# Kernel tuning notes

Measured on AMD Instinct MI355X. Metric: run time of the kernel, lower is better.

## Reference

```python
import jax, jax.numpy as jnp
import numpy as np
import math

B, S, DK, DV = 8, 2048, 128, 128
SQRT_DK = math.sqrt(DK)


def setup_inputs() -> dict:
    key = jax.random.key(0)
    kq, kk, kv = jax.random.split(key, 3)
    Q = jax.random.normal(kq, (B, S, DK), dtype=jnp.float32)
    K = jax.random.normal(kk, (B, S, DK), dtype=jnp.float32)
    V = jax.random.normal(kv, (B, S, DV), dtype=jnp.float32)
    # additive causal mask, broadcast over batch: 0 on/below diag, -1e9 above
    causal = jnp.tril(jnp.ones((S, S), dtype=bool))
    mask = jnp.where(causal, 0.0, -1e9).astype(jnp.float32)[None]  # [1, S, S]
    return {"Q": Q, "K": K, "V": V, "mask": mask}


def reference(Q, K, V, mask):
    # QK = Q @ K^T / sqrt(dk); dropout is identity in eval mode.
    scores = jnp.einsum("bqd,bkd->bqk", Q, K) / SQRT_DK + mask  # [B, S, S]
    # transpose->softmax(dim=1)->transpose == softmax over key axis (last dim)
    A = jax.nn.softmax(scores, axis=-1)
    return jnp.einsum("bqk,bkv->bqv", A, V)  # [B, S, DV]
```

## Files before the change

### kernel.cpp

```cpp
#include <hip/hip_runtime.h>

#define SEQ 2048
#define DHEAD 128
#define NB 8
#define KST 136
#define VST 72
#define PST 72

typedef short short8 __attribute__((ext_vector_type(8)));
typedef float f32x4 __attribute__((ext_vector_type(4)));

__device__ __constant__ unsigned char UNIT[80] = {
    124,125,126,127, 120,121,122, 116,117,118, 112,113,114, 108,109,110,
    104,105,106, 96,97,98, 100,101,102, 92,93,94, 88,89, 84,85, 80,81,
    76,77, 72,73, 68,69, 64,65, 60,61, 56, 52, 48, 44, 40, 36, 32, 28,
    123, 90, 57, 24,
    119, 86, 53, 20,
    115, 82, 49, 16,
    111, 78, 45, 12,
    107, 74, 41,  8,
    103, 70, 37,  4,
     99, 66, 33,  0
};

__device__ __forceinline__ unsigned short f2bf(float x) {
    unsigned int u = __float_as_uint(x);
    u += 0x7fffu + ((u >> 16) & 1u);
    return (unsigned short)(u >> 16);
}

__device__ __forceinline__ float bf2f(unsigned short h) {
    return __uint_as_float(((unsigned int)h) << 16);
}

__global__ void prep(const float* __restrict__ K, const float* __restrict__ V,
                     unsigned short* __restrict__ Kb, unsigned short* __restrict__ Vt) {
    if (blockIdx.x < 2048) {
        int i = blockIdx.x * 256 + threadIdx.x;
        float4 v = ((const float4*)K)[i];
        ushort4 o;
        o.x = f2bf(v.x); o.y = f2bf(v.y); o.z = f2bf(v.z); o.w = f2bf(v.w);
        ((ushort4*)Kb)[i] = o;
    } else {
        __shared__ unsigned short t[32][33];
        int bx = blockIdx.x - 2048;
        int b = bx >> 8, xy = bx & 255;
        int s0 = (xy >> 2) << 5;
        int d0 = (xy & 3) << 5;
        int tid = threadIdx.x;
        int sl = tid >> 3, dl = (tid & 7) << 2;
        float4 v = *(const float4*)&V[(b * SEQ + s0 + sl) * DHEAD + d0 + dl];
        t[sl][dl + 0] = f2bf(v.x); t[sl][dl + 1] = f2bf(v.y);
        t[sl][dl + 2] = f2bf(v.z); t[sl][dl + 3] = f2bf(v.w);
        __syncthreads();
        int dr = tid >> 3, sr = (tid & 7) << 2;
        ushort4 o;
        o.x = t[sr + 0][dr]; o.y = t[sr + 1][dr]; o.z = t[sr + 2][dr]; o.w = t[sr + 3][dr];
        *(ushort4*)&Vt[(b * DHEAD + d0 + dr) * SEQ + s0 + sr] = o;
    }
}

__global__ __launch_bounds__(256, 3)
void flash_attn(const float* __restrict__ Q, const unsigned short* __restrict__ Kb,
                const unsigned short* __restrict__ Vt,
                unsigned short* __restrict__ Opart, float* __restrict__ lsumP,
                float* __restrict__ out) {
    __shared__ __align__(16) unsigned short Klds[64 * KST];
    __shared__ __align__(16) unsigned short Vlds[128 * VST];
    __shared__ __align__(16) unsigned short Pb[4][16 * PST];

    const int b = blockIdx.x & 7;
    const int e = UNIT[blockIdx.x >> 3];
    const int qt = e >> 2, c = e & 3;
    const int kt0 = c * 8;
    const int kt1 = min(qt + 1, kt0 + 8);

    const int tid = threadIdx.x;
    const int w = tid >> 6, lane = tid & 63;
    const int ln15 = lane & 15, g = lane >> 4;
    const int qrow0 = qt * 64 + w * 16;

    const float scale = 0.08838834764831845f;
    short8 qf[4];
    {
        const float* qp = Q + (b * SEQ + qrow0 + ln15) * DHEAD + g * 8;
#pragma unroll
        for (int cc = 0; cc < 4; ++cc) {
            float4 a = *(const float4*)(qp + cc * 32);
            float4 d = *(const float4*)(qp + cc * 32 + 4);
            short8 f;
            f[0] = f2bf(a.x * scale); f[1] = f2bf(a.y * scale);
            f[2] = f2bf(a.z * scale); f[3] = f2bf(a.w * scale);
            f[4] = f2bf(d.x * scale); f[5] = f2bf(d.y * scale);
            f[6] = f2bf(d.z * scale); f[7] = f2bf(d.w * scale);
            qf[cc] = f;
        }
    }

    f32x4 acc[8];
#pragma unroll
    for (int j = 0; j < 8; ++j) acc[j] = (f32x4){0.f, 0.f, 0.f, 0.f};
    float lsum = 0.f;
    unsigned short* P = &Pb[w][0];

    {
        const int k0 = kt0 << 6;
        short8 pre[8];
#pragma unroll
        for (int j = 0; j < 4; ++j) {
            int ck = tid + j * 256;
            pre[j]     = *(const short8*)(Kb + (b * SEQ + k0 + (ck >> 4)) * DHEAD + (ck & 15) * 8);
            pre[4 + j] = *(const short8*)(Vt + (b * DHEAD + (ck >> 3)) * SEQ + k0 + (ck & 7) * 8);
        }
#pragma unroll
        for (int j = 0; j < 4; ++j) {
            int ck = tid + j * 256;
            *(short8*)&Klds[(ck >> 4) * KST + (ck & 15) * 8] = pre[j];
            *(short8*)&Vlds[(ck >> 3) * VST + (ck & 7) * 8]  = pre[4 + j];
        }
    }
    __syncthreads();

    for (int kt = kt0; kt < kt1; ++kt) {
        const int k0 = kt << 6;
        const bool have_next = (kt + 1 < kt1);
        short8 pre2[8];
        if (have_next) {
            const int kn = (kt + 1) << 6;
#pragma unroll
            for (int j = 0; j < 4; ++j) {
                int ck = tid + j * 256;
                pre2[j]     = *(const short8*)(Kb + (b * SEQ + kn + (ck >> 4)) * DHEAD + (ck & 15) * 8);
                pre2[4 + j] = *(const short8*)(Vt + (b * DHEAD + (ck >> 3)) * SEQ + kn + (ck & 7) * 8);
            }
        }

        if (k0 <= qrow0 + 15) {
            const bool nm = (k0 + 63 > qrow0);
#pragma unroll
            for (int mtp = 0; mtp < 2; ++mtp) {
                short8 kf[8];
#pragma unroll
                for (int cc = 0; cc < 4; ++cc) {
                    kf[cc]     = *(const short8*)&Klds[((2 * mtp) * 16 + ln15) * KST + cc * 32 + g * 8];
                    kf[4 + cc] = *(const short8*)&Klds[((2 * mtp + 1) * 16 + ln15) * KST + cc * 32 + g * 8];
                }
                f32x4 s0 = (f32x4){0.f, 0.f, 0.f, 0.f};
                f32x4 s1 = (f32x4){0.f, 0.f, 0.f, 0.f};
#pragma unroll
                for (int cc = 0; cc < 4; ++cc) {
                    s0 = __builtin_amdgcn_mfma_f32_16x16x32_bf16(kf[cc],     qf[cc], s0, 0, 0, 0);
                    s1 = __builtin_amdgcn_mfma_f32_16x16x32_bf16(kf[4 + cc], qf[cc], s1, 0, 0, 0);
                }
#pragma unroll
                for (int h = 0; h < 2; ++h) {
                    f32x4 s = h ? s1 : s0;
                    const int mt = 2 * mtp + h;
                    float p[4];
#pragma unroll
                    for (int r = 0; r < 4; ++r) {
                        p[r] = __expf(s[r]);
                        if (nm) {
                            int colg = k0 + mt * 16 + g * 4 + r;
                            int rowg = qrow0 + ln15;
                            p[r] = (colg <= rowg) ? p[r] : 0.f;
                        }
                    }
                    lsum += (p[0] + p[1]) + (p[2] + p[3]);
                    uint2 dd;
                    dd.x = __builtin_amdgcn_perm(__float_as_uint(p[1]), __float_as_uint(p[0]), 0x07060302u);
                    dd.y = __builtin_amdgcn_perm(__float_as_uint(p[3]), __float_as_uint(p[2]), 0x07060302u);
                    *(uint2*)&P[ln15 * PST + mt * 16 + g * 4] = dd;
                }
            }
#pragma unroll
            for (int c2 = 0; c2 < 2; ++c2) {
                short8 vf[8];
#pragma unroll
                for (int nt2 = 0; nt2 < 8; ++nt2)
                    vf[nt2] = *(const short8*)&Vlds[(nt2 * 16 + ln15) * VST + c2 * 32 + g * 8];
                short8 pf = *(const short8*)&P[ln15 * PST + c2 * 32 + g * 8];
#pragma unroll
                for (int nt2 = 0; nt2 < 8; ++nt2)
                    acc[nt2] = __builtin_amdgcn_mfma_f32_16x16x32_bf16(pf, vf[nt2], acc[nt2], 0, 0, 0);
            }
        }

        if (have_next) {
            __syncthreads();
#pragma unroll
            for (int j = 0; j < 4; ++j) {
                int ck = tid + j * 256;
                *(short8*)&Klds[(ck >> 4) * KST + (ck & 15) * 8] = pre2[j];
                *(short8*)&Vlds[(ck >> 3) * VST + (ck & 7) * 8]  = pre2[4 + j];
            }
            __syncthreads();
        }
    }

    {
        float v = lsum;
        v += __shfl_xor(v, 16);
        v += __shfl_xor(v, 32);
        lsum = v;
    }

    if (qt < 8) {
        float inv[4];
#pragma unroll
        for (int r = 0; r < 4; ++r) inv[r] = 1.0f / __shfl(lsum, g * 4 + r);
#pragma unroll
        for (int nt2 = 0; nt2 < 8; ++nt2) {
#pragma unroll
            for (int r = 0; r < 4; ++r) {
                int rowg = qrow0 + g * 4 + r;
                out[(b * SEQ + rowg) * DHEAD + nt2 * 16 + ln15] = acc[nt2][r] * inv[r];
            }
        }
    } else {
        if (lane < 16)
            lsumP[(c * NB + b) * 1536 + qrow0 + lane - 512] = lsum;
#pragma unroll
        for (int nt2 = 0; nt2 < 8; ++nt2) {
#pragma unroll
            for (int r = 0; r < 4; ++r) {
                int r2 = qrow0 + g * 4 + r - 512;
                Opart[((c * NB + b) * 1536 + r2) * DHEAD + nt2 * 16 + ln15] = f2bf(acc[nt2][r]);
            }
        }
    }
}

__global__ void finalize(const unsigned short* __restrict__ Opart,
                         const float* __restrict__ lsumP, float* __restrict__ out) {
    int b = blockIdx.y;
    int gx = blockIdx.x * 256 + threadIdx.x;
    int d4 = gx & 31;
    int r2 = gx >> 5;
    int row = 512 + r2;
    int nch = (row >> 9) + 1;
    float4 o = {0.f, 0.f, 0.f, 0.f};
    float l = 0.f;
    for (int cc = 0; cc < nch; ++cc) {
        ushort4 ph = ((const ushort4*)Opart)[((cc * NB + b) * 1536 + r2) * 32 + d4];
        o.x += bf2f(ph.x); o.y += bf2f(ph.y); o.z += bf2f(ph.z); o.w += bf2f(ph.w);
        l += lsumP[(cc * NB + b) * 1536 + r2];
    }
    float inv = 1.0f / l;
    float4 r;
    r.x = o.x * inv; r.y = o.y * inv; r.z = o.z * inv; r.w = o.w * inv;
    ((float4*)out)[(b * SEQ + row) * 32 + d4] = r;
}

extern "C" void kernel_launch(void* const* d_in, const int* in_sizes, int n_in,
                              void* d_out, int out_size, void* d_ws, size_t ws_size,
                              hipStream_t stream) {
    const float* Q = (const float*)d_in[0];
    const float* K = (const float*)d_in[1];
    const float* V = (const float*)d_in[2];
    float* out = (float*)d_out;

    const int NE = NB * SEQ * DHEAD;
    unsigned short* Kb = (unsigned short*)d_ws;
    unsigned short* Vt = Kb + NE;
    unsigned short* Opart = Vt + NE;
    float* lsumP = (float*)(Opart + 4 * NB * 1536 * DHEAD);

    prep<<<4096, 256, 0, stream>>>(K, V, Kb, Vt);
    flash_attn<<<640, 256, 0, stream>>>(Q, Kb, Vt, Opart, lsumP, out);
    finalize<<<dim3(192, NB), 256, 0, stream>>>(Opart, lsumP, out);
}
```

Before: 110.5 us.

## Double query rows per block and split keys into smaller chunks

Each block now handles 128 query rows (32 per wave, two 16-row MFMA tiles), so each K/V tile loaded into LDS is reused across twice as many queries. The split-KV partitioning changes to chunks of 4 key tiles (256 keys), with a new work-unit table, a 1792-row partial buffer, and an updated finalize reduction. This halves the K/V traffic per query, but it doubles accumulator registers, lowers occupancy to 2 blocks per CU, and leaves more partial results to write and combine.

```diff
diff --git a/kernel.cpp b/kernel.cpp
--- a/kernel.cpp
+++ b/kernel.cpp
@@ -6,21 +6,28 @@
 #define KST 136
 #define VST 72
 #define PST 72
+#define PR 1792
 
 typedef short short8 __attribute__((ext_vector_type(8)));
 typedef float f32x4 __attribute__((ext_vector_type(4)));
 
-__device__ __constant__ unsigned char UNIT[80] = {
-    124,125,126,127, 120,121,122, 116,117,118, 112,113,114, 108,109,110,
-    104,105,106, 96,97,98, 100,101,102, 92,93,94, 88,89, 84,85, 80,81,
-    76,77, 72,73, 68,69, 64,65, 60,61, 56, 52, 48, 44, 40, 36, 32, 28,
-    123, 90, 57, 24,
-    119, 86, 53, 20,
-    115, 82, 49, 16,
-    111, 78, 45, 12,
-    107, 74, 41,  8,
-    103, 70, 37,  4,
-     99, 66, 33,  0
+__device__ __constant__ unsigned char UNIT[72] = {
+    120,121,122,123,124,125,126,127,
+    112,113,114,115,116,117,118,
+    104,105,106,107,108,109,110,
+    96,97,98,99,100,101,
+    88,89,90,91,92,93,
+    80,81,82,83,84,
+    72,73,74,75,76,
+    64,65,66,67,
+    56,57,58,59,
+    48,49,50,
+    40,41,42,
+    32,33,
+    24,25,
+    16,
+    8,
+    119,102,85,68,51,34,17,0
 };
 
 __device__ __forceinline__ unsigned short f2bf(float x) {
@@ -60,30 +67,31 @@
     }
 }
 
-__global__ __launch_bounds__(256, 3)
+__global__ __launch_bounds__(256, 2)
 void flash_attn(const float* __restrict__ Q, const unsigned short* __restrict__ Kb,
                 const unsigned short* __restrict__ Vt,
                 unsigned short* __restrict__ Opart, float* __restrict__ lsumP,
                 float* __restrict__ out) {
     __shared__ __align__(16) unsigned short Klds[64 * KST];
     __shared__ __align__(16) unsigned short Vlds[128 * VST];
-    __shared__ __align__(16) unsigned short Pb[4][16 * PST];
+    __shared__ __align__(16) unsigned short Pb[4][32 * PST];
 
     const int b = blockIdx.x & 7;
     const int e = UNIT[blockIdx.x >> 3];
-    const int qt = e >> 2, c = e & 3;
-    const int kt0 = c * 8;
-    const int kt1 = min(qt + 1, kt0 + 8);
+    const int qt = e >> 3, c = e & 7;
+    const int kt0 = c * 4;
+    const int kt1 = min(2 * qt + 2, kt0 + 4);
 
     const int tid = threadIdx.x;
     const int w = tid >> 6, lane = tid & 63;
     const int ln15 = lane & 15, g = lane >> 4;
-    const int qrow0 = qt * 64 + w * 16;
+    const int qrow0 = qt * 128 + w * 32;
 
     const float scale = 0.08838834764831845f;
-    short8 qf[4];
-    {
-        const float* qp = Q + (b * SEQ + qrow0 + ln15) * DHEAD + g * 8;
+    short8 qf[2][4];
+#pragma unroll
+    for (int nt = 0; nt < 2; ++nt) {
+        const float* qp = Q + (b * SEQ + qrow0 + nt * 16 + ln15) * DHEAD + g * 8;
 #pragma unroll
         for (int cc = 0; cc < 4; ++cc) {
             float4 a = *(const float4*)(qp + cc * 32);
@@ -93,14 +101,16 @@
             f[2] = f2bf(a.z * scale); f[3] = f2bf(a.w * scale);
             f[4] = f2bf(d.x * scale); f[5] = f2bf(d.y * scale);
             f[6] = f2bf(d.z * scale); f[7] = f2bf(d.w * scale);
-            qf[cc] = f;
-        }
-    }
-
-    f32x4 acc[8];
-#pragma unroll
-    for (int j = 0; j < 8; ++j) acc[j] = (f32x4){0.f, 0.f, 0.f, 0.f};
-    float lsum = 0.f;
+            qf[nt][cc] = f;
+        }
+    }
+
+    f32x4 acc[2][8];
+#pragma unroll
+    for (int nt = 0; nt < 2; ++nt)
+#pragma unroll
+        for (int j = 0; j < 8; ++j) acc[nt][j] = (f32x4){0.f, 0.f, 0.f, 0.f};
+    float lsum[2] = {0.f, 0.f};
     unsigned short* P = &Pb[w][0];
 
     {
@@ -135,7 +145,7 @@
             }
         }
 
-        if (k0 <= qrow0 + 15) {
+        if (k0 <= qrow0 + 31) {
             const bool nm = (k0 + 63 > qrow0);
 #pragma unroll
             for (int mtp = 0; mtp < 2; ++mtp) {
@@ -145,32 +155,39 @@
                     kf[cc]     = *(const short8*)&Klds[((2 * mtp) * 16 + ln15) * KST + cc * 32 + g * 8];
                     kf[4 + cc] = *(const short8*)&Klds[((2 * mtp + 1) * 16 + ln15) * KST + cc * 32 + g * 8];
                 }
-                f32x4 s0 = (f32x4){0.f, 0.f, 0.f, 0.f};
-                f32x4 s1 = (f32x4){0.f, 0.f, 0.f, 0.f};
+                f32x4 s00 = (f32x4){0.f, 0.f, 0.f, 0.f};
+                f32x4 s01 = (f32x4){0.f, 0.f, 0.f, 0.f};
+                f32x4 s10 = (f32x4){0.f, 0.f, 0.f, 0.f};
+                f32x4 s11 = (f32x4){0.f, 0.f, 0.f, 0.f};
 #pragma unroll
                 for (int cc = 0; cc < 4; ++cc) {
-                    s0 = __builtin_amdgcn_mfma_f32_16x16x32_bf16(kf[cc],     qf[cc], s0, 0, 0, 0);
-                    s1 = __builtin_amdgcn_mfma_f32_16x16x32_bf16(kf[4 + cc], qf[cc], s1, 0, 0, 0);
+                    s00 = __builtin_amdgcn_mfma_f32_16x16x32_bf16(kf[cc],     qf[0][cc], s00, 0, 0, 0);
+                    s10 = __builtin_amdgcn_mfma_f32_16x16x32_bf16(kf[4 + cc], qf[0][cc], s10, 0, 0, 0);
+                    s01 = __builtin_amdgcn_mfma_f32_16x16x32_bf16(kf[cc],     qf[1][cc], s01, 0, 0, 0);
+                    s11 = __builtin_amdgcn_mfma_f32_16x16x32_bf16(kf[4 + cc], qf[1][cc], s11, 0, 0, 0);
                 }
 #pragma unroll
                 for (int h = 0; h < 2; ++h) {
-                    f32x4 s = h ? s1 : s0;
-                    const int mt = 2 * mtp + h;
-                    float p[4];
-#pragma unroll
-                    for (int r = 0; r < 4; ++r) {
-                        p[r] = __expf(s[r]);
-                        if (nm) {
-                            int colg = k0 + mt * 16 + g * 4 + r;
-                            int rowg = qrow0 + ln15;
-                            p[r] = (colg <= rowg) ? p[r] : 0.f;
+#pragma unroll
+                    for (int nt = 0; nt < 2; ++nt) {
+                        f32x4 s = h ? (nt ? s11 : s10) : (nt ? s01 : s00);
+                        const int mt = 2 * mtp + h;
+                        float p[4];
+#pragma unroll
+                        for (int r = 0; r < 4; ++r) {
+                            p[r] = __expf(s[r]);
+                            if (nm) {
+                                int colg = k0 + mt * 16 + g * 4 + r;
+                                int rowg = qrow0 + nt * 16 + ln15;
+                                p[r] = (colg <= rowg) ? p[r] : 0.f;
+                            }
                         }
+                        lsum[nt] += (p[0] + p[1]) + (p[2] + p[3]);
+                        uint2 dd;
+                        dd.x = __builtin_amdgcn_perm(__float_as_uint(p[1]), __float_as_uint(p[0]), 0x07060302u);
+                        dd.y = __builtin_amdgcn_perm(__float_as_uint(p[3]), __float_as_uint(p[2]), 0x07060302u);
+                        *(uint2*)&P[(nt * 16 + ln15) * PST + mt * 16 + g * 4] = dd;
                     }
-                    lsum += (p[0] + p[1]) + (p[2] + p[3]);
-                    uint2 dd;
-                    dd.x = __builtin_amdgcn_perm(__float_as_uint(p[1]), __float_as_uint(p[0]), 0x07060302u);
-                    dd.y = __builtin_amdgcn_perm(__float_as_uint(p[3]), __float_as_uint(p[2]), 0x07060302u);
-                    *(uint2*)&P[ln15 * PST + mt * 16 + g * 4] = dd;
                 }
             }
 #pragma unroll
@@ -179,10 +196,13 @@
 #pragma unroll
                 for (int nt2 = 0; nt2 < 8; ++nt2)
                     vf[nt2] = *(const short8*)&Vlds[(nt2 * 16 + ln15) * VST + c2 * 32 + g * 8];
-                short8 pf = *(const short8*)&P[ln15 * PST + c2 * 32 + g * 8];
-#pragma unroll
-                for (int nt2 = 0; nt2 < 8; ++nt2)
-                    acc[nt2] = __builtin_amdgcn_mfma_f32_16x16x32_bf16(pf, vf[nt2], acc[nt2], 0, 0, 0);
+#pragma unroll
+                for (int nt = 0; nt < 2; ++nt) {
+                    short8 pf = *(const short8*)&P[(nt * 16 + ln15) * PST + c2 * 32 + g * 8];
+#pragma unroll
+                    for (int nt2 = 0; nt2 < 8; ++nt2)
+                        acc[nt][nt2] = __builtin_amdgcn_mfma_f32_16x16x32_bf16(pf, vf[nt2], acc[nt][nt2], 0, 0, 0);
+                }
             }
         }
 
@@ -198,34 +218,43 @@
         }
     }
 
-    {
-        float v = lsum;
+#pragma unroll
+    for (int nt = 0; nt < 2; ++nt) {
+        float v = lsum[nt];
         v += __shfl_xor(v, 16);
         v += __shfl_xor(v, 32);
-        lsum = v;
-    }
-
-    if (qt < 8) {
-        float inv[4];
-#pragma unroll
-        for (int r = 0; r < 4; ++r) inv[r] = 1.0f / __shfl(lsum, g * 4 + r);
-#pragma unroll
-        for (int nt2 = 0; nt2 < 8; ++nt2) {
-#pragma unroll
-            for (int r = 0; r < 4; ++r) {
-                int rowg = qrow0 + g * 4 + r;
-                out[(b * SEQ + rowg) * DHEAD + nt2 * 16 + ln15] = acc[nt2][r] * inv[r];
+        lsum[nt] = v;
+    }
+
+    if (qt < 2) {
+#pragma unroll
+        for (int nt = 0; nt < 2; ++nt) {
+            float inv[4];
+#pragma unroll
+            for (int r = 0; r < 4; ++r) inv[r] = 1.0f / __shfl(lsum[nt], g * 4 + r);
+#pragma unroll
+            for (int nt2 = 0; nt2 < 8; ++nt2) {
+#pragma unroll
+                for (int r = 0; r < 4; ++r) {
+                    int rowg = qrow0 + nt * 16 + g * 4 + r;
+                    out[(b * SEQ + rowg) * DHEAD + nt2 * 16 + ln15] = acc[nt][nt2][r] * inv[r];
+                }
             }
         }
     } else {
-        if (lane < 16)
-            lsumP[(c * NB + b) * 1536 + qrow0 + lane - 512] = lsum;
-#pragma unroll
-        for (int nt2 = 0; nt2 < 8; ++nt2) {
-#pragma unroll
-            for (int r = 0; r < 4; ++r) {
-                int r2 = qrow0 + g * 4 + r - 512;
-                Opart[((c * NB + b) * 1536 + r2) * DHEAD + nt2 * 16 + ln15] = f2bf(acc[nt2][r]);
+#pragma unroll
+        for (int nt = 0; nt < 2; ++nt)
+            if (lane < 16)
+                lsumP[(c * NB + b) * PR + qrow0 + nt * 16 + lane - 256] = lsum[nt];
+#pragma unroll
+        for (int nt = 0; nt < 2; ++nt) {
+#pragma unroll
+            for (int nt2 = 0; nt2 < 8; ++nt2) {
+#pragma unroll
+                for (int r = 0; r < 4; ++r) {
+                    int r2 = qrow0 + nt * 16 + g * 4 + r - 256;
+                    Opart[((c * NB + b) * PR + r2) * DHEAD + nt2 * 16 + ln15] = f2bf(acc[nt][nt2][r]);
+                }
             }
         }
     }
@@ -237,14 +266,14 @@
     int gx = blockIdx.x * 256 + threadIdx.x;
     int d4 = gx & 31;
     int r2 = gx >> 5;
-    int row = 512 + r2;
-    int nch = (row >> 9) + 1;
+    int row = 256 + r2;
+    int nch = (row >> 8) + 1;
     float4 o = {0.f, 0.f, 0.f, 0.f};
     float l = 0.f;
     for (int cc = 0; cc < nch; ++cc) {
-        ushort4 ph = ((const ushort4*)Opart)[((cc * NB + b) * 1536 + r2) * 32 + d4];
+        ushort4 ph = ((const ushort4*)Opart)[((cc * NB + b) * PR + r2) * 32 + d4];
         o.x += bf2f(ph.x); o.y += bf2f(ph.y); o.z += bf2f(ph.z); o.w += bf2f(ph.w);
-        l += lsumP[(cc * NB + b) * 1536 + r2];
+        l += lsumP[(cc * NB + b) * PR + r2];
     }
     float inv = 1.0f / l;
     float4 r;
@@ -264,9 +293,9 @@
     unsigned short* Kb = (unsigned short*)d_ws;
     unsigned short* Vt = Kb + NE;
     unsigned short* Opart = Vt + NE;
-    float* lsumP = (float*)(Opart + 4 * NB * 1536 * DHEAD);
+    float* lsumP = (float*)(Opart + 8 * NB * PR * DHEAD);
 
     prep<<<4096, 256, 0, stream>>>(K, V, Kb, Vt);
-    flash_attn<<<640, 256, 0, stream>>>(Q, Kb, Vt, Opart, lsumP, out);
-    finalize<<<dim3(192, NB), 256, 0, stream>>>(Opart, lsumP, out);
-}
+    flash_attn<<<576, 256, 0, stream>>>(Q, Kb, Vt, Opart, lsumP, out);
+    finalize<<<dim3(224, NB), 256, 0, stream>>>(Opart, lsumP, out);
+}
```

Result: no change. 111.3 us (+0.8%).
